# Kernel optimization log

Measured on AMD Instinct MI355X. Metric: run time of the kernel, lower is better.

## Reference

```python
import jax, jax.numpy as jnp
from jax import lax
import numpy as np

B, T, K = 128, 256, 50
START_TAG, END_TAG = 48, 49  # from tag_map['<start>'], tag_map['<end>']


def setup_inputs() -> dict:
    key = jax.random.key(0)
    k1, k2, k3 = jax.random.split(key, 3)
    scores = jax.random.normal(k1, (B, T, K, K), dtype=jnp.float32)
    targets = jax.random.randint(k2, (B, T), 0, K * K)
    lengths = jax.random.randint(k3, (B,), 1, T + 1)
    return {"scores": scores, "targets": targets, "lengths": lengths, "tmap_correct": 0}


def reference(scores, targets, lengths, tmap_correct):
    b, t_pad, k, _ = scores.shape
    # gold score: gather flat (prev_tag, cur_tag) indices, mask out padding
    flat = scores.reshape(b, t_pad, k * k)
    scores_at_targets = jnp.take_along_axis(flat, targets[:, :, None], axis=2)[..., 0]  # [B, T]
    time_mask = jnp.arange(t_pad)[None, :] < lengths[:, None]  # [B, T]
    gold_score = jnp.sum(jnp.where(time_mask, scores_at_targets, 0.0))

    # forward (all-paths) recursion; equivalent to the sorted/batch_size_t loop:
    # each sequence's alpha is only updated while t < length.
    alpha0 = jnp.where((lengths > 0)[:, None], scores[:, 0, START_TAG, :], 0.0)  # [B, K]

    scores_tbkk = jnp.swapaxes(scores, 0, 1)[1:]  # [T-1, B, K, K]
    ts = jnp.arange(1, t_pad)

    def step(alpha, inp):
        t, s_t = inp  # s_t: [B, K, K]
        new_alpha = jax.scipy.special.logsumexp(s_t + alpha[:, :, None], axis=1)  # [B, K]
        alpha = jnp.where((t < lengths)[:, None], new_alpha, alpha)
        return alpha, None

    alpha, _ = lax.scan(step, alpha0, (ts, scores_tbkk))
    all_paths_scores = jnp.sum(alpha[:, END_TAG])
    return (all_paths_scores - gold_score) / b
```

## Files before the change

kernel.cpp:

```cpp
#include <hip/hip_runtime.h>

#define K_TAGS 50
#define T_MAX 256
#define START_TAG 48
#define END_TAG 49
#define LOG2E 1.4426950408889634f
#define LN2 0.6931471805599453f
#define KK 2500

#define EXP2F(x) __builtin_amdgcn_exp2f(x)
#define LOG2F(x) __builtin_amdgcn_logf(x)

__device__ __forceinline__ float rdlane(float v, int i) {
    return __int_as_float(__builtin_amdgcn_readlane(__float_as_int(v), i));
}

__device__ __forceinline__ void barrier_lds() {
    __builtin_amdgcn_sched_barrier(0);
    __builtin_amdgcn_s_waitcnt(0xC07F);
    __builtin_amdgcn_s_barrier();
    __builtin_amdgcn_sched_barrier(0);
}

__global__ __launch_bounds__(256, 1) void crf_fwd_kernel(
    const float* __restrict__ scores, const int* __restrict__ targets,
    const int* __restrict__ lengths, float* __restrict__ accum,
    float* __restrict__ uv)
{
    const int b    = blockIdx.x >> 1;
    const int dir  = blockIdx.x & 1;
    const int tid  = threadIdx.x;
    const int wave = tid >> 6;
    const int lane = tid & 63;
    const int len  = lengths[b];
    const float* __restrict__ sp = scores + (size_t)b * T_MAX * KK;
    const int jc = (lane < K_TAGS) ? lane : (K_TAGS - 1);

    __shared__ float pbuf[2][4 * 64];

    const int m = (len - 2) / 2;
    int count = dir ? (len - 2 - m) : m;
    if (count < 0) count = 0;

    if (dir == 0) {
        float g = 0.f;
        if (tid < len) g = sp[(size_t)tid * KK + targets[b * T_MAX + tid]];
        #pragma unroll
        for (int off = 32; off; off >>= 1) g += __shfl_down(g, off, 64);
        if (lane == 0) atomicAdd(&accum[1], g);
    }

    float L, M;
    if (dir == 0) {
        float bc = sp[START_TAG * K_TAGS + jc] * LOG2E;
        M = rdlane(bc, 0);
        L = EXP2F(bc - M);
    } else {
        M = 0.f;
        if (len >= 2)
            L = EXP2F(sp[(size_t)(len - 1) * KK + jc * K_TAGS + END_TAG] * LOG2E);
        else
            L = (jc == END_TAG) ? 1.f : 0.f;
    }

    const int rb = 13 * wave;

    if (count > 0) {
        auto tof = [&](int s) {
            int ss = (s <= count) ? s : count;
            return dir ? (len - 1 - ss) : ss;
        };

        float S[4][13], P[2][13];

        auto loadset = [&](int set, int s) {
            const float* base = sp + (size_t)tof(s) * KK + rb * K_TAGS + jc;
            #pragma unroll
            for (int r = 0; r < 13; ++r) S[set][r] = base[r * K_TAGS];
        };
        auto expset = [&](int pd, int ss) {
            #pragma unroll
            for (int r = 0; r < 13; ++r) {
                float e = EXP2F(S[ss][r] * LOG2E);
                if (r >= 11 && rb + r >= K_TAGS) e = 0.f;
                P[pd][r] = e;
            }
        };

        #pragma unroll
        for (int q = 1; q <= 4; ++q) loadset(q & 3, q);
        expset(1, 1);

        for (int s0 = 1; s0 <= count; s0 += 4) {
            #pragma unroll
            for (int k = 0; k < 4; ++k) {
                const int  st  = s0 + k;
                const int  SS  = (k + 1) & 3;
                const int  SSn = (k + 2) & 3;
                const int  PP  = (k + 1) & 1;
                const int  PPn = k & 1;
                const bool live = (st <= count);

                if (live) loadset(SS, st + 4);

                if (live) {
                    float a0 = 0.f, a1 = 0.f, a2 = 0.f;
                    #pragma unroll
                    for (int r = 0; r < 13; r += 3) {
                        a0 = __builtin_fmaf(P[PP][r], rdlane(L, rb + r), a0);
                        if (r + 1 < 13)
                            a1 = __builtin_fmaf(P[PP][r + 1], rdlane(L, rb + r + 1), a1);
                        if (r + 2 < 13)
                            a2 = __builtin_fmaf(P[PP][r + 2], rdlane(L, rb + r + 2), a2);
                    }
                    if (lane < K_TAGS)
                        pbuf[PP][(wave << 6) + lane] = (a0 + a1) + a2;
                }

                expset(PPn, SSn);

                barrier_lds();

                if (live) {
                    float p0 = pbuf[PP][jc];
                    float p1 = pbuf[PP][64 + jc];
                    float p2 = pbuf[PP][128 + jc];
                    float p3 = pbuf[PP][192 + jc];
                    float sum = (p0 + p1) + (p2 + p3);
                    int   ei = (__float_as_int(rdlane(sum, 0)) >> 23) & 0xFF;
                    float scale = __int_as_float((254 - ei) << 23);
                    L = sum * scale;
                    M += (float)(ei - 127);
                }
            }
        }
    }

    if (wave == 0) {
        float* w = uv + (size_t)(dir ? (gridDim.x >> 1) + b : b) * 64;
        if (lane < K_TAGS) w[lane] = L;
        if (lane == 0)     w[K_TAGS] = M;
    }
}

__global__ void combine_kernel(const float* __restrict__ uv,
                               float* __restrict__ accum, int B)
{
    const int b = blockIdx.x, lane = threadIdx.x;
    const float* U = uv + (size_t)b * 64;
    const float* V = uv + (size_t)(B + b) * 64;
    float prod = (lane < K_TAGS) ? U[lane] * V[lane] : 0.f;
    #pragma unroll
    for (int off = 32; off; off >>= 1) prod += __shfl_down(prod, off, 64);
    if (lane == 0) {
        float z = (U[K_TAGS] + V[K_TAGS] + LOG2F(prod)) * LN2;
        atomicAdd(&accum[0], z);
    }
}

__global__ void finalize_kernel(const float* __restrict__ accum,
                                float* __restrict__ out, float invB)
{
    out[0] = (accum[0] - accum[1]) * invB;
}

extern "C" void kernel_launch(void* const* d_in, const int* in_sizes, int n_in,
                              void* d_out, int out_size, void* d_ws, size_t ws_size,
                              hipStream_t stream)
{
    const float* scores  = (const float*)d_in[0];
    const int*   targets = (const int*)d_in[1];
    const int*   lengths = (const int*)d_in[2];
    const int B = in_sizes[2];

    float* accum = (float*)d_ws;
    float* uv    = (float*)d_ws + 16;
    hipMemsetAsync(accum, 0, 2 * sizeof(float), stream);
    crf_fwd_kernel<<<2 * B, 256, 0, stream>>>(scores, targets, lengths, accum, uv);
    combine_kernel<<<B, 64, 0, stream>>>(uv, accum, B);
    finalize_kernel<<<1, 1, 0, stream>>>(accum, (float*)d_out, 1.0f / (float)B);
}
```

Measured before the change: 421.1 us.

## Stage exponentiated score matrices in LDS via coalesced float4 loads

Each block now loads the whole K×K score matrix for a timestep with contiguous float4 loads of 12 floats per thread. It exponentiates each element once and writes it to a double-buffered LDS tile, where waves read their 13-row slices. The backward direction reads the tile transposed. This replaces the per-wave strided scalar register loads and the redundant exponentiation done by padded lanes, and it keeps a three-stage register prefetch ring. The cost is 24 KB of extra LDS, LDS reads with possible bank conflicts on the transposed path, and loads that run past the 2500-element matrix, which could go out of bounds on the last timestep of the last batch.

```diff
diff --git a/kernel.cpp b/kernel.cpp
--- a/kernel.cpp
+++ b/kernel.cpp
@@ -7,6 +7,7 @@
 #define LOG2E 1.4426950408889634f
 #define LN2 0.6931471805599453f
 #define KK 2500
+#define LDSN 3072
 
 #define EXP2F(x) __builtin_amdgcn_exp2f(x)
 #define LOG2F(x) __builtin_amdgcn_logf(x)
@@ -34,9 +35,12 @@
     const int lane = tid & 63;
     const int len  = lengths[b];
     const float* __restrict__ sp = scores + (size_t)b * T_MAX * KK;
-    const int jc = (lane < K_TAGS) ? lane : (K_TAGS - 1);
+    const int jc  = (lane < K_TAGS) ? lane : (K_TAGS - 1);
+    const int rb  = 13 * wave;
+    const int lin = tid * 12;
 
-    __shared__ float pbuf[2][4 * 64];
+    __shared__ float Gds[2][LDSN];
+    __shared__ float pbuf[2][256];
 
     const int m = (len - 2) / 2;
     int count = dir ? (len - 2 - m) : m;
@@ -63,75 +67,76 @@
             L = (jc == END_TAG) ? 1.f : 0.f;
     }
 
-    const int rb = 13 * wave;
+    if (count > 0) {
+        float4 R4[3][3];
 
-    if (count > 0) {
-        auto tof = [&](int s) {
-            int ss = (s <= count) ? s : count;
-            return dir ? (len - 1 - ss) : ss;
+        auto issue_loads = [&](float4 (&dst)[3], int q) {
+            int ss = (q <= count) ? q : count;
+            int tt = dir ? (len - 1 - ss) : ss;
+            const float4* gp = (const float4*)(sp + (size_t)tt * KK + lin);
+            dst[0] = gp[0]; dst[1] = gp[1]; dst[2] = gp[2];
         };
-
-        float S[4][13], P[2][13];
-
-        auto loadset = [&](int set, int s) {
-            const float* base = sp + (size_t)tof(s) * KK + rb * K_TAGS + jc;
+        auto exp_write = [&](float* gb, const float4 (&src)[3]) {
+            float4* gw = (float4*)(gb + lin);
             #pragma unroll
-            for (int r = 0; r < 13; ++r) S[set][r] = base[r * K_TAGS];
-        };
-        auto expset = [&](int pd, int ss) {
-            #pragma unroll
-            for (int r = 0; r < 13; ++r) {
-                float e = EXP2F(S[ss][r] * LOG2E);
-                if (r >= 11 && rb + r >= K_TAGS) e = 0.f;
-                P[pd][r] = e;
+            for (int k = 0; k < 3; ++k) {
+                float4 v = src[k], w;
+                w.x = EXP2F(v.x * LOG2E); w.y = EXP2F(v.y * LOG2E);
+                w.z = EXP2F(v.z * LOG2E); w.w = EXP2F(v.w * LOG2E);
+                gw[k] = w;
             }
         };
 
-        #pragma unroll
-        for (int q = 1; q <= 4; ++q) loadset(q & 3, q);
-        expset(1, 1);
+        issue_loads(R4[1], 1);
+        issue_loads(R4[2], 2);
+        issue_loads(R4[0], 3);
+        __builtin_amdgcn_sched_barrier(0);
+        exp_write(Gds[1], R4[1]);
+        barrier_lds();
 
-        for (int s0 = 1; s0 <= count; s0 += 4) {
+        int s = 1;
+        while (s <= count) {
             #pragma unroll
-            for (int k = 0; k < 4; ++k) {
-                const int  st  = s0 + k;
-                const int  SS  = (k + 1) & 3;
-                const int  SSn = (k + 2) & 3;
-                const int  PP  = (k + 1) & 1;
-                const int  PPn = k & 1;
-                const bool live = (st <= count);
-
-                if (live) loadset(SS, st + 4);
+            for (int u = 0; u < 6; ++u) {
+                const int PLd = (1 + u) % 3;
+                const int PEx = (2 + u) % 3;
+                const int PWr = u & 1;
+                const int PRd = (1 + u) & 1;
+                const bool live = (s <= count);
 
                 if (live) {
-                    float a0 = 0.f, a1 = 0.f, a2 = 0.f;
-                    #pragma unroll
-                    for (int r = 0; r < 13; r += 3) {
-                        a0 = __builtin_fmaf(P[PP][r], rdlane(L, rb + r), a0);
-                        if (r + 1 < 13)
-                            a1 = __builtin_fmaf(P[PP][r + 1], rdlane(L, rb + r + 1), a1);
-                        if (r + 2 < 13)
-                            a2 = __builtin_fmaf(P[PP][r + 2], rdlane(L, rb + r + 2), a2);
+                    issue_loads(R4[PLd], s + 3);
+                    exp_write(Gds[PWr], R4[PEx]);
+                    {
+                        const float* g = Gds[PRd];
+                        float a0 = 0.f, a1 = 0.f, a2 = 0.f;
+                        #pragma unroll
+                        for (int r = 0; r < 13; ++r) {
+                            int idx = dir ? (jc * K_TAGS + rb + r)
+                                          : ((rb + r) * K_TAGS + jc);
+                            float gv = g[idx];
+                            if (r >= 11 && rb + r >= K_TAGS) gv = 0.f;
+                            float lv = rdlane(L, rb + r);
+                            if ((r % 3) == 0)      a0 = __builtin_fmaf(gv, lv, a0);
+                            else if ((r % 3) == 1) a1 = __builtin_fmaf(gv, lv, a1);
+                            else                   a2 = __builtin_fmaf(gv, lv, a2);
+                        }
+                        pbuf[PRd][(wave << 6) + lane] = (a0 + a1) + a2;
                     }
-                    if (lane < K_TAGS)
-                        pbuf[PP][(wave << 6) + lane] = (a0 + a1) + a2;
                 }
-
-                expset(PPn, SSn);
-
                 barrier_lds();
-
                 if (live) {
-                    float p0 = pbuf[PP][jc];
-                    float p1 = pbuf[PP][64 + jc];
-                    float p2 = pbuf[PP][128 + jc];
-                    float p3 = pbuf[PP][192 + jc];
+                    float p0 = pbuf[PRd][jc];
+                    float p1 = pbuf[PRd][64 + jc];
+                    float p2 = pbuf[PRd][128 + jc];
+                    float p3 = pbuf[PRd][192 + jc];
                     float sum = (p0 + p1) + (p2 + p3);
                     int   ei = (__float_as_int(rdlane(sum, 0)) >> 23) & 0xFF;
                     float scale = __int_as_float((254 - ei) << 23);
                     L = sum * scale;
                     M += (float)(ei - 127);
                 }
+                ++s;
             }
         }
     }
```

Measured after the change: 431.8 us. 1.03x slower.

## Restructure bidirectional CRF recursion with LDS transpose and reduced renormalization

Applied to the files above, without the earlier changes.

Splits the forward and backward halves into separate code paths. The backward direction now transposes exp-scores through a padded LDS buffer instead of using a different access pattern, and the work split moves to about 9/16 forward. The partial-sum buffer becomes interleaved so each lane reads all four wave partials with one float4 load, and renormalization happens only every fourth step. Loads and exps for later steps are moved after the barrier to overlap with the wait. The trade-offs are extra LDS traffic and barrier work on the backward path, plus a risk of overflow from the less frequent rescaling.

```diff
diff --git a/kernel.cpp b/kernel.cpp
--- a/kernel.cpp
+++ b/kernel.cpp
@@ -7,6 +7,7 @@
 #define LOG2E 1.4426950408889634f
 #define LN2 0.6931471805599453f
 #define KK 2500
+#define GPAD 53
 
 #define EXP2F(x) __builtin_amdgcn_exp2f(x)
 #define LOG2F(x) __builtin_amdgcn_logf(x)
@@ -35,10 +36,12 @@
     const int len  = lengths[b];
     const float* __restrict__ sp = scores + (size_t)b * T_MAX * KK;
     const int jc = (lane < K_TAGS) ? lane : (K_TAGS - 1);
-
-    __shared__ float pbuf[2][4 * 64];
-
-    const int m = (len - 2) / 2;
+    const int rb = 13 * wave;
+
+    __shared__ float Gt[2][K_TAGS * GPAD];
+    __shared__ __align__(16) float pbuf[2][256];
+
+    const int m = (len >= 2) ? (((len - 2) * 9) >> 4) : 0;
     int count = dir ? (len - 2 - m) : m;
     if (count < 0) count = 0;
 
@@ -57,80 +60,131 @@
         L = EXP2F(bc - M);
     } else {
         M = 0.f;
-        if (len >= 2)
-            L = EXP2F(sp[(size_t)(len - 1) * KK + jc * K_TAGS + END_TAG] * LOG2E);
-        else
-            L = (jc == END_TAG) ? 1.f : 0.f;
-    }
-
-    const int rb = 13 * wave;
+        L = (len >= 2)
+            ? EXP2F(sp[(size_t)(len - 1) * KK + jc * K_TAGS + END_TAG] * LOG2E)
+            : ((jc == END_TAG) ? 1.f : 0.f);
+    }
 
     if (count > 0) {
+        float S[4][13];
+        float P[2][13];
         auto tof = [&](int s) {
             int ss = (s <= count) ? s : count;
             return dir ? (len - 1 - ss) : ss;
         };
-
-        float S[4][13], P[2][13];
-
         auto loadset = [&](int set, int s) {
-            const float* base = sp + (size_t)tof(s) * KK + rb * K_TAGS + jc;
+            const float* p = sp + (size_t)tof(s) * KK + rb * K_TAGS + jc;
             #pragma unroll
-            for (int r = 0; r < 13; ++r) S[set][r] = base[r * K_TAGS];
+            for (int r = 0; r < 13; ++r) S[set][r] = p[r * K_TAGS];
         };
-        auto expset = [&](int pd, int ss) {
-            #pragma unroll
-            for (int r = 0; r < 13; ++r) {
-                float e = EXP2F(S[ss][r] * LOG2E);
-                if (r >= 11 && rb + r >= K_TAGS) e = 0.f;
-                P[pd][r] = e;
+
+        const int nseg = (count + 3) >> 2;
+
+        if (dir == 0) {
+            auto expset = [&](int pd, int set) {
+                #pragma unroll
+                for (int r = 0; r < 13; ++r) {
+                    float e = EXP2F(S[set][r] * LOG2E);
+                    if (r >= 11 && rb + r >= K_TAGS) e = 0.f;
+                    P[pd][r] = e;
+                }
+            };
+            loadset(1, 1); loadset(2, 2); loadset(3, 3); loadset(0, 4);
+            expset(1, 1);
+            int st = 1;
+            for (int g = 0; g < nseg; ++g) {
+                #pragma unroll
+                for (int u = 0; u < 4; ++u) {
+                    const int  PP = (1 + u) & 1;
+                    const bool live = (st <= count);
+                    if (live) {
+                        float a0 = 0.f, a1 = 0.f, a2 = 0.f;
+                        #pragma unroll
+                        for (int r = 0; r < 13; r += 3) {
+                            a0 = __builtin_fmaf(P[PP][r], rdlane(L, rb + r), a0);
+                            if (r + 1 < 13)
+                                a1 = __builtin_fmaf(P[PP][r + 1], rdlane(L, rb + r + 1), a1);
+                            if (r + 2 < 13)
+                                a2 = __builtin_fmaf(P[PP][r + 2], rdlane(L, rb + r + 2), a2);
+                        }
+                        if (lane < K_TAGS) pbuf[PP][jc * 4 + wave] = (a0 + a1) + a2;
+                    }
+                    barrier_lds();
+                    if (live) {
+                        float4 pv = *(const float4*)&pbuf[PP][jc * 4];
+                        loadset((1 + u) & 3, st + 4);
+                        expset(u & 1, (2 + u) & 3);
+                        float sum = (pv.x + pv.y) + (pv.z + pv.w);
+                        if ((st & 3) == 0) {
+                            int ei = (__float_as_int(rdlane(sum, 0)) >> 23) & 0xFF;
+                            float scale = __int_as_float((254 - ei) << 23);
+                            L = sum * scale;
+                            M += (float)(ei - 127);
+                        } else L = sum;
+                    }
+                    ++st;
+                }
             }
-        };
-
-        #pragma unroll
-        for (int q = 1; q <= 4; ++q) loadset(q & 3, q);
-        expset(1, 1);
-
-        for (int s0 = 1; s0 <= count; s0 += 4) {
-            #pragma unroll
-            for (int k = 0; k < 4; ++k) {
-                const int  st  = s0 + k;
-                const int  SS  = (k + 1) & 3;
-                const int  SSn = (k + 2) & 3;
-                const int  PP  = (k + 1) & 1;
-                const int  PPn = k & 1;
-                const bool live = (st <= count);
-
-                if (live) loadset(SS, st + 4);
-
-                if (live) {
-                    float a0 = 0.f, a1 = 0.f, a2 = 0.f;
-                    #pragma unroll
-                    for (int r = 0; r < 13; r += 3) {
-                        a0 = __builtin_fmaf(P[PP][r], rdlane(L, rb + r), a0);
-                        if (r + 1 < 13)
-                            a1 = __builtin_fmaf(P[PP][r + 1], rdlane(L, rb + r + 1), a1);
-                        if (r + 2 < 13)
-                            a2 = __builtin_fmaf(P[PP][r + 2], rdlane(L, rb + r + 2), a2);
-                    }
-                    if (lane < K_TAGS)
-                        pbuf[PP][(wave << 6) + lane] = (a0 + a1) + a2;
-                }
-
-                expset(PPn, SSn);
-
-                barrier_lds();
-
-                if (live) {
-                    float p0 = pbuf[PP][jc];
-                    float p1 = pbuf[PP][64 + jc];
-                    float p2 = pbuf[PP][128 + jc];
-                    float p3 = pbuf[PP][192 + jc];
-                    float sum = (p0 + p1) + (p2 + p3);
-                    int   ei = (__float_as_int(rdlane(sum, 0)) >> 23) & 0xFF;
-                    float scale = __int_as_float((254 - ei) << 23);
-                    L = sum * scale;
-                    M += (float)(ei - 127);
+        } else {
+            auto expE = [&](int set) {
+                #pragma unroll
+                for (int r = 0; r < 13; ++r) P[0][r] = EXP2F(S[set][r] * LOG2E);
+            };
+            auto writeGt = [&](int gpar) {
+                float* g = Gt[gpar];
+                #pragma unroll
+                for (int r = 0; r < 13; ++r)
+                    if (rb + r < K_TAGS && lane < K_TAGS)
+                        g[(rb + r) * GPAD + jc] = P[0][r];
+            };
+            auto readR = [&](int gpar) {
+                const float* g = Gt[gpar];
+                #pragma unroll
+                for (int r = 0; r < 13; ++r)
+                    if (rb + r < K_TAGS) P[1][r] = g[jc * GPAD + rb + r];
+            };
+            loadset(1, 1); loadset(2, 2); loadset(3, 3); loadset(0, 4);
+            expE(1);
+            writeGt(1);
+            loadset(1, 5);
+            expE(2);
+            barrier_lds();
+            readR(1);
+            int st = 1;
+            for (int g = 0; g < nseg; ++g) {
+                #pragma unroll
+                for (int u = 0; u < 4; ++u) {
+                    const int  PP = (1 + u) & 1;
+                    const bool live = (st <= count);
+                    if (live) {
+                        float a0 = 0.f, a1 = 0.f, a2 = 0.f;
+                        #pragma unroll
+                        for (int r = 0; r < 13; r += 3) {
+                            if (rb + r < K_TAGS)
+                                a0 = __builtin_fmaf(P[1][r], rdlane(L, rb + r), a0);
+                            if (r + 1 < 13 && rb + r + 1 < K_TAGS)
+                                a1 = __builtin_fmaf(P[1][r + 1], rdlane(L, rb + r + 1), a1);
+                            if (r + 2 < 13 && rb + r + 2 < K_TAGS)
+                                a2 = __builtin_fmaf(P[1][r + 2], rdlane(L, rb + r + 2), a2);
+                        }
+                        if (lane < K_TAGS) pbuf[PP][jc * 4 + wave] = (a0 + a1) + a2;
+                        writeGt(u & 1);
+                    }
+                    barrier_lds();
+                    if (live) {
+                        float4 pv = *(const float4*)&pbuf[PP][jc * 4];
+                        loadset((2 + u) & 3, st + 5);
+                        readR(u & 1);
+                        expE((3 + u) & 3);
+                        float sum = (pv.x + pv.y) + (pv.z + pv.w);
+                        if ((st & 3) == 0) {
+                            int ei = (__float_as_int(rdlane(sum, 0)) >> 23) & 0xFF;
+                            float scale = __int_as_float((254 - ei) << 23);
+                            L = sum * scale;
+                            M += (float)(ei - 127);
+                        } else L = sum;
+                    }
+                    ++st;
                 }
             }
         }
```

New measurement: 460.1 us. 9.3% more time.
